# Optimization experiments

Hardware: AMD Instinct MI355X
Metric: run time of the kernel (lower is better)

Reference implementation:

```python
import jax, jax.numpy as jnp
import numpy as np

MIN_RES, MAX_RES, NUM_LOD, BAND_WIDTH = 16, 512, 8, 19
CODEBOOK_SIZE = 2 ** BAND_WIDTH  # 524288
_b = np.exp((np.log(MAX_RES) - np.log(MIN_RES)) / (NUM_LOD - 1))
LODS = [int(1 + np.floor(MIN_RES * _b ** l)) for l in range(NUM_LOD)]
SIZES = [min(CODEBOOK_SIZE, r ** 3) for r in LODS]
PRIMES = (1, 2654435761, 805459861)  # Instant-NGP spatial hash primes
N_PTS = 2_000_000

# corner offsets of the unit cube, [8,3]
_OFFS = np.array([[(i >> 2) & 1, (i >> 1) & 1, i & 1] for i in range(8)], dtype=np.int32)


def _hash_interp(p01, table, res, size):
    """Hashed trilinear interpolation for one LOD. p01:[N,3] in [0,1], table:[size]."""
    x = p01 * (res - 1)                                   # [N,3]
    c0 = jnp.clip(jnp.floor(x), 0, res - 2).astype(jnp.int32)
    frac = x - c0.astype(jnp.float32)                     # [N,3]
    offs = jnp.asarray(_OFFS)                             # [8,3]
    corners = (c0[:, None, :] + offs[None]).astype(jnp.uint32)  # [N,8,3]
    h = (corners[..., 0] * jnp.uint32(PRIMES[0])
         ^ corners[..., 1] * jnp.uint32(PRIMES[1])
         ^ corners[..., 2] * jnp.uint32(PRIMES[2]))
    idx = (h % jnp.uint32(size)).astype(jnp.int32)        # [N,8]
    feats = table[idx]                                    # [N,8] gather
    offf = offs.astype(jnp.float32)
    # trilinear weights: prod_d (frac if offset else 1-frac)
    w = jnp.prod(frac[:, None, :] * offf + (1.0 - frac[:, None, :]) * (1.0 - offf), axis=-1)
    return jnp.sum(w * feats, axis=-1)                    # [N]


def setup_inputs() -> dict:
    key = jax.random.key(0)
    k1, k2 = jax.random.split(key)
    pts = jax.random.uniform(k1, (N_PTS, 3), jnp.float32) * 2.0 - 1.0  # [-1,1]^3
    codebook = jax.random.normal(k2, (NUM_LOD, CODEBOOK_SIZE, 1), jnp.float32) * 0.01
    return {"pts": pts, "codebook": codebook}


def reference(pts, codebook):
    p01 = pts / 2.0 + 0.5                                  # normalize to [0,1]
    out = jnp.zeros(pts.shape[0], jnp.float32)
    for i, res in enumerate(LODS):                         # small static loop over LODs
        table = codebook[i, : SIZES[i], 0]                 # static slice -> actual table size
        out = out + _hash_interp(p01, table, res, SIZES[i])
    return out[:, None]                                    # [N, feat_dim=1]
```

## Files before the change

### kernel.cpp

```cpp
#include <hip/hip_runtime.h>
#include <math.h>


static constexpr unsigned CB_STRIDE = 524288u;
static constexpr int S0 = 4913;
static constexpr int S1 = 19683;
static constexpr int WO2 = 0;
static constexpr int WO3 = 85184;
static constexpr int WO4 = 443104;
static constexpr int WO5 = 967392;
static constexpr int WO6 = 1491680;
static constexpr int WO7 = 2015968;
static constexpr size_t WS_NEED_BYTES = 2540256u * 2u;

__device__ __forceinline__ unsigned short f32_to_bf16_rne(float f) {
    unsigned u = __float_as_uint(f);
    u = (u + 0x7FFFu + ((u >> 16) & 1u)) >> 16;
    return (unsigned short)u;
}
__device__ __forceinline__ float bf16_to_f32(unsigned short s) {
    return __uint_as_float(((unsigned)s) << 16);
}

struct I8 { unsigned a0, a1, a2, a3, a4, a5, a6, a7; };
struct R8 { unsigned short v0, v1, v2, v3, v4, v5, v6, v7; };
struct W3 { float x, y, z; };

template <unsigned SIZE, bool POW2>
__device__ __forceinline__ I8 idx8(float p01x, float p01y, float p01z, int res, W3& fr)
{
    const float rm1 = (float)(res - 1);
    float xx = p01x * rm1, yy = p01y * rm1, zz = p01z * rm1;
    const float cmax = (float)(res - 2);
    float fx = fminf(fmaxf(floorf(xx), 0.0f), cmax);
    float fy = fminf(fmaxf(floorf(yy), 0.0f), cmax);
    float fz = fminf(fmaxf(floorf(zz), 0.0f), cmax);
    fr.x = xx - fx; fr.y = yy - fy; fr.z = zz - fz;
    const unsigned ix = (unsigned)(int)fx;
    const unsigned iy = (unsigned)(int)fy;
    const unsigned iz = (unsigned)(int)fz;

    const unsigned hx0 = ix;
    const unsigned hx1 = ix + 1u;
    const unsigned hy0 = iy * 2654435761u;
    const unsigned hy1 = hy0 + 2654435761u;
    const unsigned hz0 = iz * 805459861u;
    const unsigned hz1 = hz0 + 805459861u;

    unsigned v0 = hx0 ^ hy0 ^ hz0;
    unsigned v1 = hx0 ^ hy0 ^ hz1;
    unsigned v2 = hx0 ^ hy1 ^ hz0;
    unsigned v3 = hx0 ^ hy1 ^ hz1;
    unsigned v4 = hx1 ^ hy0 ^ hz0;
    unsigned v5 = hx1 ^ hy0 ^ hz1;
    unsigned v6 = hx1 ^ hy1 ^ hz0;
    unsigned v7 = hx1 ^ hy1 ^ hz1;

    if (POW2) {
        const unsigned m = SIZE - 1u;
        v0 &= m; v1 &= m; v2 &= m; v3 &= m; v4 &= m; v5 &= m; v6 &= m; v7 &= m;
    } else {
        v0 %= SIZE; v1 %= SIZE; v2 %= SIZE; v3 %= SIZE;
        v4 %= SIZE; v5 %= SIZE; v6 %= SIZE; v7 %= SIZE;
    }
    I8 o; o.a0 = v0; o.a1 = v1; o.a2 = v2; o.a3 = v3;
          o.a4 = v4; o.a5 = v5; o.a6 = v6; o.a7 = v7;
    return o;
}

__device__ __forceinline__ R8 gather8(const unsigned short* __restrict__ t, I8 o)
{
    R8 r;
    r.v0 = t[o.a0]; r.v1 = t[o.a1]; r.v2 = t[o.a2]; r.v3 = t[o.a3];
    r.v4 = t[o.a4]; r.v5 = t[o.a5]; r.v6 = t[o.a6]; r.v7 = t[o.a7];
    return r;
}

__device__ __forceinline__ float acc8(R8 r, W3 f)
{
    const float wx1 = f.x, wx0 = 1.0f - f.x;
    const float wy1 = f.y, wy0 = 1.0f - f.y;
    const float wz1 = f.z, wz0 = 1.0f - f.z;
    const float w00 = wy0 * wz0, w01 = wy0 * wz1;
    const float w10 = wy1 * wz0, w11 = wy1 * wz1;
    const float sx0 = bf16_to_f32(r.v0) * w00 + bf16_to_f32(r.v1) * w01
                    + bf16_to_f32(r.v2) * w10 + bf16_to_f32(r.v3) * w11;
    const float sx1 = bf16_to_f32(r.v4) * w00 + bf16_to_f32(r.v5) * w01
                    + bf16_to_f32(r.v6) * w10 + bf16_to_f32(r.v7) * w11;
    return wx0 * sx0 + wx1 * sx1;
}

__global__ __launch_bounds__(1024)
void HashGrid_convert_kernel(const float* __restrict__ codebook,
                             unsigned short* __restrict__ ws)
{
    const int lod = blockIdx.y;
    const int sizes[6] = {85184, 357911, 524288, 524288, 524288, 524288};
    const int offs[6]  = {WO2, WO3, WO4, WO5, WO6, WO7};
    const int idx = blockIdx.x * 1024 + threadIdx.x;
    if (idx < sizes[lod])
        ws[offs[lod] + idx] = f32_to_bf16_rne(codebook[(unsigned)(lod + 2) * CB_STRIDE + idx]);
}

__global__ __launch_bounds__(1024, 4)
void HashGrid_88278757802387_kernel(const float* __restrict__ pts,
                                    const float* __restrict__ codebook,
                                    const unsigned short* __restrict__ ws,
                                    float* __restrict__ out,
                                    int n, int res7)
{
    __shared__ unsigned short sm[S0 + S1];
    for (int j = threadIdx.x; j < S0 + S1; j += 1024)
        sm[j] = f32_to_bf16_rne(j < S0 ? codebook[j] : codebook[CB_STRIDE + (j - S0)]);
    __syncthreads();

    const int i = blockIdx.x * 1024 + threadIdx.x;
    if (i >= n) return;

    const float p01x = pts[3 * i + 0] * 0.5f + 0.5f;
    const float p01y = pts[3 * i + 1] * 0.5f + 0.5f;
    const float p01z = pts[3 * i + 2] * 0.5f + 0.5f;

    W3 fA, fB, fC, fD, fE, fF, fL0, fL1;
    I8 oA = idx8<85184u,  false>(p01x, p01y, p01z, 44,   fA);
    I8 oB = idx8<357911u, false>(p01x, p01y, p01z, 71,   fB);
    I8 oC = idx8<524288u, true >(p01x, p01y, p01z, 116,  fC);
    I8 oD = idx8<524288u, true >(p01x, p01y, p01z, 191,  fD);
    I8 oE = idx8<524288u, true >(p01x, p01y, p01z, 313,  fE);
    I8 oF = idx8<524288u, true >(p01x, p01y, p01z, res7, fF);

    R8 rA = gather8(ws + WO2, oA);
    R8 rB = gather8(ws + WO3, oB);
    R8 rC = gather8(ws + WO4, oC);
    R8 rD = gather8(ws + WO5, oD);
    R8 rE = gather8(ws + WO6, oE);
    R8 rF = gather8(ws + WO7, oF);

    I8 oL0 = idx8<4913u,  false>(p01x, p01y, p01z, 17, fL0);
    I8 oL1 = idx8<19683u, false>(p01x, p01y, p01z, 27, fL1);
    R8 rL0 = gather8(sm, oL0);
    R8 rL1 = gather8(sm + S0, oL1);
    float acc = acc8(rL0, fL0) + acc8(rL1, fL1);

    acc += acc8(rA, fA);
    acc += acc8(rB, fB);
    acc += acc8(rC, fC);
    acc += acc8(rD, fD);
    acc += acc8(rE, fE);
    acc += acc8(rF, fF);

    out[i] = acc;
}

__global__ __launch_bounds__(1024, 4)
void HashGrid_fallback_kernel(const float* __restrict__ pts,
                              const float* __restrict__ codebook,
                              float* __restrict__ out,
                              int n, int res7)
{
    const int i = blockIdx.x * 1024 + threadIdx.x;
    if (i >= n) return;
    const float p01x = pts[3 * i + 0] * 0.5f + 0.5f;
    const float p01y = pts[3 * i + 1] * 0.5f + 0.5f;
    const float p01z = pts[3 * i + 2] * 0.5f + 0.5f;
    float acc = 0.0f;
    const int      reslist[8]  = {17, 27, 44, 71, 116, 191, 313, res7};
    const unsigned sizelist[8] = {4913u, 19683u, 85184u, 357911u, 524288u, 524288u, 524288u, 524288u};
    for (int l = 0; l < 8; ++l) {
        const int res = reslist[l];
        const unsigned size = sizelist[l];
        const float rm1 = (float)(res - 1);
        float xx = p01x * rm1, yy = p01y * rm1, zz = p01z * rm1;
        float fx = fminf(fmaxf(floorf(xx), 0.0f), (float)(res - 2));
        float fy = fminf(fmaxf(floorf(yy), 0.0f), (float)(res - 2));
        float fz = fminf(fmaxf(floorf(zz), 0.0f), (float)(res - 2));
        const float frx = xx - fx, fry = yy - fy, frz = zz - fz;
        const unsigned ix = (unsigned)(int)fx, iy = (unsigned)(int)fy, iz = (unsigned)(int)fz;
        const unsigned hy0 = iy * 2654435761u, hy1 = hy0 + 2654435761u;
        const unsigned hz0 = iz * 805459861u,  hz1 = hz0 + 805459861u;
        const unsigned o0 = (ix ^ hy0 ^ hz0) % size,      o1 = (ix ^ hy0 ^ hz1) % size;
        const unsigned o2 = (ix ^ hy1 ^ hz0) % size,      o3 = (ix ^ hy1 ^ hz1) % size;
        const unsigned o4 = ((ix+1u) ^ hy0 ^ hz0) % size, o5 = ((ix+1u) ^ hy0 ^ hz1) % size;
        const unsigned o6 = ((ix+1u) ^ hy1 ^ hz0) % size, o7 = ((ix+1u) ^ hy1 ^ hz1) % size;
        const float* tab = codebook + (unsigned)l * CB_STRIDE;
        const float wx1 = frx, wx0 = 1.0f - frx;
        const float wy1 = fry, wy0 = 1.0f - fry;
        const float wz1 = frz, wz0 = 1.0f - frz;
        const float w00 = wy0*wz0, w01 = wy0*wz1, w10 = wy1*wz0, w11 = wy1*wz1;
        acc += wx0 * (tab[o0]*w00 + tab[o1]*w01 + tab[o2]*w10 + tab[o3]*w11)
             + wx1 * (tab[o4]*w00 + tab[o5]*w01 + tab[o6]*w10 + tab[o7]*w11);
    }
    out[i] = acc;
}

extern "C" void kernel_launch(void* const* d_in, const int* in_sizes, int n_in,
                              void* d_out, int out_size, void* d_ws, size_t ws_size,
                              hipStream_t stream)
{
    const float* pts      = (const float*)d_in[0];
    const float* codebook = (const float*)d_in[1];
    float* out            = (float*)d_out;
    const int n = in_sizes[0] / 3;

    const double b = exp((log(512.0) - log(16.0)) / 7.0);
    const int res7 = (int)(1.0 + floor(16.0 * pow(b, 7.0)));

    const bool use_ws = (d_ws != nullptr) && (ws_size >= WS_NEED_BYTES);
    const int blocks = (n + 1023) / 1024;

    if (use_ws) {
        unsigned short* ws = (unsigned short*)d_ws;
        hipLaunchKernelGGL(HashGrid_convert_kernel, dim3(512, 6), dim3(1024),
                           0, stream, codebook, ws);
        hipLaunchKernelGGL(HashGrid_88278757802387_kernel, dim3(blocks), dim3(1024),
                           0, stream, pts, codebook, ws, out, n, res7);
    } else {
        hipLaunchKernelGGL(HashGrid_fallback_kernel, dim3(blocks), dim3(1024),
                           0, stream, pts, codebook, out, n, res7);
    }
}
```

Before: 406.5 us.

## Drop shared-memory tables for coarse LODs, interleave gather and accumulate, use 256-thread blocks

Moves the two coarse LOD tables from per-block shared memory into the bf16 workspace, which the convert kernel now fills for all eight levels. This removes the per-block shared-memory fill and its barrier. The kernel now does each LOD's hash, gather and accumulate inline instead of issuing all 48 workspace gathers before any accumulation, which cuts live registers but may expose more memory latency per level. The block size drops from 1024 to 256 threads, giving finer scheduling granularity.

```diff
diff --git a/kernel.cpp b/kernel.cpp
--- a/kernel.cpp
+++ b/kernel.cpp
@@ -3,15 +3,15 @@
 
 
 static constexpr unsigned CB_STRIDE = 524288u;
-static constexpr int S0 = 4913;
-static constexpr int S1 = 19683;
-static constexpr int WO2 = 0;
-static constexpr int WO3 = 85184;
-static constexpr int WO4 = 443104;
-static constexpr int WO5 = 967392;
-static constexpr int WO6 = 1491680;
-static constexpr int WO7 = 2015968;
-static constexpr size_t WS_NEED_BYTES = 2540256u * 2u;
+static constexpr int WO0 = 0;
+static constexpr int WO1 = 4928;
+static constexpr int WO2 = 24640;
+static constexpr int WO3 = 109824;
+static constexpr int WO4 = 467744;
+static constexpr int WO5 = 992032;
+static constexpr int WO6 = 1516320;
+static constexpr int WO7 = 2040608;
+static constexpr size_t WS_NEED_BYTES = 2564896u * 2u;
 
 __device__ __forceinline__ unsigned short f32_to_bf16_rne(float f) {
     unsigned u = __float_as_uint(f);
@@ -22,12 +22,10 @@
     return __uint_as_float(((unsigned)s) << 16);
 }
 
-struct I8 { unsigned a0, a1, a2, a3, a4, a5, a6, a7; };
-struct R8 { unsigned short v0, v1, v2, v3, v4, v5, v6, v7; };
-struct W3 { float x, y, z; };
-
 template <unsigned SIZE, bool POW2>
-__device__ __forceinline__ I8 idx8(float p01x, float p01y, float p01z, int res, W3& fr)
+__device__ __forceinline__ float lod_interp(float p01x, float p01y, float p01z,
+                                            const unsigned short* __restrict__ t,
+                                            int res)
 {
     const float rm1 = (float)(res - 1);
     float xx = p01x * rm1, yy = p01y * rm1, zz = p01z * rm1;
@@ -35,7 +33,7 @@
     float fx = fminf(fmaxf(floorf(xx), 0.0f), cmax);
     float fy = fminf(fmaxf(floorf(yy), 0.0f), cmax);
     float fz = fminf(fmaxf(floorf(zz), 0.0f), cmax);
-    fr.x = xx - fx; fr.y = yy - fy; fr.z = zz - fz;
+    const float frx = xx - fx, fry = yy - fy, frz = zz - fz;
     const unsigned ix = (unsigned)(int)fx;
     const unsigned iy = (unsigned)(int)fy;
     const unsigned iz = (unsigned)(int)fz;
@@ -63,30 +61,23 @@
         v0 %= SIZE; v1 %= SIZE; v2 %= SIZE; v3 %= SIZE;
         v4 %= SIZE; v5 %= SIZE; v6 %= SIZE; v7 %= SIZE;
     }
-    I8 o; o.a0 = v0; o.a1 = v1; o.a2 = v2; o.a3 = v3;
-          o.a4 = v4; o.a5 = v5; o.a6 = v6; o.a7 = v7;
-    return o;
-}
 
-__device__ __forceinline__ R8 gather8(const unsigned short* __restrict__ t, I8 o)
-{
-    R8 r;
-    r.v0 = t[o.a0]; r.v1 = t[o.a1]; r.v2 = t[o.a2]; r.v3 = t[o.a3];
-    r.v4 = t[o.a4]; r.v5 = t[o.a5]; r.v6 = t[o.a6]; r.v7 = t[o.a7];
-    return r;
-}
+    const float t000 = bf16_to_f32(t[v0]);
+    const float t001 = bf16_to_f32(t[v1]);
+    const float t010 = bf16_to_f32(t[v2]);
+    const float t011 = bf16_to_f32(t[v3]);
+    const float t100 = bf16_to_f32(t[v4]);
+    const float t101 = bf16_to_f32(t[v5]);
+    const float t110 = bf16_to_f32(t[v6]);
+    const float t111 = bf16_to_f32(t[v7]);
 
-__device__ __forceinline__ float acc8(R8 r, W3 f)
-{
-    const float wx1 = f.x, wx0 = 1.0f - f.x;
-    const float wy1 = f.y, wy0 = 1.0f - f.y;
-    const float wz1 = f.z, wz0 = 1.0f - f.z;
+    const float wx1 = frx, wx0 = 1.0f - frx;
+    const float wy1 = fry, wy0 = 1.0f - fry;
+    const float wz1 = frz, wz0 = 1.0f - frz;
     const float w00 = wy0 * wz0, w01 = wy0 * wz1;
     const float w10 = wy1 * wz0, w11 = wy1 * wz1;
-    const float sx0 = bf16_to_f32(r.v0) * w00 + bf16_to_f32(r.v1) * w01
-                    + bf16_to_f32(r.v2) * w10 + bf16_to_f32(r.v3) * w11;
-    const float sx1 = bf16_to_f32(r.v4) * w00 + bf16_to_f32(r.v5) * w01
-                    + bf16_to_f32(r.v6) * w10 + bf16_to_f32(r.v7) * w11;
+    const float sx0 = t000 * w00 + t001 * w01 + t010 * w10 + t011 * w11;
+    const float sx1 = t100 * w00 + t101 * w01 + t110 * w10 + t111 * w11;
     return wx0 * sx0 + wx1 * sx1;
 }
 
@@ -95,70 +86,46 @@
                              unsigned short* __restrict__ ws)
 {
     const int lod = blockIdx.y;
-    const int sizes[6] = {85184, 357911, 524288, 524288, 524288, 524288};
-    const int offs[6]  = {WO2, WO3, WO4, WO5, WO6, WO7};
+    const int sizes[8] = {4913, 19683, 85184, 357911, 524288, 524288, 524288, 524288};
+    const int offs[8]  = {WO0, WO1, WO2, WO3, WO4, WO5, WO6, WO7};
     const int idx = blockIdx.x * 1024 + threadIdx.x;
     if (idx < sizes[lod])
-        ws[offs[lod] + idx] = f32_to_bf16_rne(codebook[(unsigned)(lod + 2) * CB_STRIDE + idx]);
+        ws[offs[lod] + idx] = f32_to_bf16_rne(codebook[(unsigned)lod * CB_STRIDE + idx]);
 }
 
-__global__ __launch_bounds__(1024, 4)
+__global__ __launch_bounds__(256, 4)
 void HashGrid_88278757802387_kernel(const float* __restrict__ pts,
-                                    const float* __restrict__ codebook,
                                     const unsigned short* __restrict__ ws,
                                     float* __restrict__ out,
                                     int n, int res7)
 {
-    __shared__ unsigned short sm[S0 + S1];
-    for (int j = threadIdx.x; j < S0 + S1; j += 1024)
-        sm[j] = f32_to_bf16_rne(j < S0 ? codebook[j] : codebook[CB_STRIDE + (j - S0)]);
-    __syncthreads();
-
-    const int i = blockIdx.x * 1024 + threadIdx.x;
+    const int i = blockIdx.x * 256 + threadIdx.x;
     if (i >= n) return;
 
     const float p01x = pts[3 * i + 0] * 0.5f + 0.5f;
     const float p01y = pts[3 * i + 1] * 0.5f + 0.5f;
     const float p01z = pts[3 * i + 2] * 0.5f + 0.5f;
 
-    W3 fA, fB, fC, fD, fE, fF, fL0, fL1;
-    I8 oA = idx8<85184u,  false>(p01x, p01y, p01z, 44,   fA);
-    I8 oB = idx8<357911u, false>(p01x, p01y, p01z, 71,   fB);
-    I8 oC = idx8<524288u, true >(p01x, p01y, p01z, 116,  fC);
-    I8 oD = idx8<524288u, true >(p01x, p01y, p01z, 191,  fD);
-    I8 oE = idx8<524288u, true >(p01x, p01y, p01z, 313,  fE);
-    I8 oF = idx8<524288u, true >(p01x, p01y, p01z, res7, fF);
-
-    R8 rA = gather8(ws + WO2, oA);
-    R8 rB = gather8(ws + WO3, oB);
-    R8 rC = gather8(ws + WO4, oC);
-    R8 rD = gather8(ws + WO5, oD);
-    R8 rE = gather8(ws + WO6, oE);
-    R8 rF = gather8(ws + WO7, oF);
-
-    I8 oL0 = idx8<4913u,  false>(p01x, p01y, p01z, 17, fL0);
-    I8 oL1 = idx8<19683u, false>(p01x, p01y, p01z, 27, fL1);
-    R8 rL0 = gather8(sm, oL0);
-    R8 rL1 = gather8(sm + S0, oL1);
-    float acc = acc8(rL0, fL0) + acc8(rL1, fL1);
-
-    acc += acc8(rA, fA);
-    acc += acc8(rB, fB);
-    acc += acc8(rC, fC);
-    acc += acc8(rD, fD);
-    acc += acc8(rE, fE);
-    acc += acc8(rF, fF);
+    float acc = 0.0f;
+    acc += lod_interp<4913u,   false>(p01x, p01y, p01z, ws + WO0, 17);
+    acc += lod_interp<19683u,  false>(p01x, p01y, p01z, ws + WO1, 27);
+    acc += lod_interp<85184u,  false>(p01x, p01y, p01z, ws + WO2, 44);
+    acc += lod_interp<357911u, false>(p01x, p01y, p01z, ws + WO3, 71);
+    acc += lod_interp<524288u, true >(p01x, p01y, p01z, ws + WO4, 116);
+    acc += lod_interp<524288u, true >(p01x, p01y, p01z, ws + WO5, 191);
+    acc += lod_interp<524288u, true >(p01x, p01y, p01z, ws + WO6, 313);
+    acc += lod_interp<524288u, true >(p01x, p01y, p01z, ws + WO7, res7);
 
     out[i] = acc;
 }
 
-__global__ __launch_bounds__(1024, 4)
+__global__ __launch_bounds__(256, 4)
 void HashGrid_fallback_kernel(const float* __restrict__ pts,
                               const float* __restrict__ codebook,
                               float* __restrict__ out,
                               int n, int res7)
 {
-    const int i = blockIdx.x * 1024 + threadIdx.x;
+    const int i = blockIdx.x * 256 + threadIdx.x;
     if (i >= n) return;
     const float p01x = pts[3 * i + 0] * 0.5f + 0.5f;
     const float p01y = pts[3 * i + 1] * 0.5f + 0.5f;
@@ -206,16 +173,16 @@
     const int res7 = (int)(1.0 + floor(16.0 * pow(b, 7.0)));
 
     const bool use_ws = (d_ws != nullptr) && (ws_size >= WS_NEED_BYTES);
-    const int blocks = (n + 1023) / 1024;
+    const int blocks = (n + 255) / 256;
 
     if (use_ws) {
         unsigned short* ws = (unsigned short*)d_ws;
-        hipLaunchKernelGGL(HashGrid_convert_kernel, dim3(512, 6), dim3(1024),
+        hipLaunchKernelGGL(HashGrid_convert_kernel, dim3(512, 8), dim3(1024),
                            0, stream, codebook, ws);
-        hipLaunchKernelGGL(HashGrid_88278757802387_kernel, dim3(blocks), dim3(1024),
-                           0, stream, pts, codebook, ws, out, n, res7);
+        hipLaunchKernelGGL(HashGrid_88278757802387_kernel, dim3(blocks), dim3(256),
+                           0, stream, pts, ws, out, n, res7);
     } else {
-        hipLaunchKernelGGL(HashGrid_fallback_kernel, dim3(blocks), dim3(1024),
+        hipLaunchKernelGGL(HashGrid_fallback_kernel, dim3(blocks), dim3(256),
                            0, stream, pts, codebook, out, n, res7);
     }
 }
```

Measured after the change: 430.8 us. 1.06x slower.
